# Performance work log

Hardware: AMD Instinct MI355X
Metric: run time of the kernel (lower is better)

Reference implementation:

```python
import jax, jax.numpy as jnp
import numpy as np

N_NODES = 50000
N_EDGES = 500000
IN_FEATS = 64
H_FEATS = 128
NUM_CLASSES = 4
NUM_GRAPHS = 8
NODES_PER_GRAPH = N_NODES // NUM_GRAPHS


def setup_inputs() -> dict:
    key = jax.random.key(0)
    ks = jax.random.split(key, 12)
    in_feat = jax.random.normal(ks[0], (N_NODES, IN_FEATS), dtype=jnp.float32)
    e_weight = jax.random.uniform(ks[1], (N_EDGES,), dtype=jnp.float32)
    src = jax.random.randint(ks[2], (N_EDGES,), 0, N_NODES)
    dst = jax.random.randint(ks[3], (N_EDGES,), 0, N_NODES)
    batch_num_nodes = jnp.full((NUM_GRAPHS,), NODES_PER_GRAPH, dtype=jnp.int64)
    target_node = jax.random.randint(ks[4], (NUM_GRAPHS,), 0, NODES_PER_GRAPH)
    # Glorot-style init for GraphConv weights, zero bias (DGL defaults)
    def glorot(k, fan_in, fan_out):
        s = jnp.sqrt(6.0 / (fan_in + fan_out))
        return jax.random.uniform(k, (fan_in, fan_out), minval=-s, maxval=s, dtype=jnp.float32)
    W1 = glorot(ks[5], IN_FEATS, H_FEATS)
    b1 = jnp.zeros((H_FEATS,), dtype=jnp.float32)
    W2 = glorot(ks[6], H_FEATS, H_FEATS)
    b2 = jnp.zeros((H_FEATS,), dtype=jnp.float32)
    W3 = glorot(ks[7], H_FEATS, NUM_CLASSES)
    b3 = jnp.zeros((NUM_CLASSES,), dtype=jnp.float32)
    return {"in_feat": in_feat, "e_weight": e_weight, "src": src, "dst": dst,
            "batch_num_nodes": batch_num_nodes, "target_node": target_node,
            "W1": W1, "b1": b1, "W2": W2, "b2": b2, "W3": W3, "b3": b3}


def _graph_conv(h, src, dst, e_weight, W, b, out_norm, in_norm, n_nodes):
    # DGL GraphConv, norm='both', with per-edge weights:
    # h_src scaled by out_deg^-1/2, weighted sum over edges into dst,
    # scaled by in_deg^-1/2, then dense transform + bias.
    h = h * out_norm[:, None]
    msg = h[src] * e_weight[:, None]           # [E, d] gather + scale
    agg = jax.ops.segment_sum(msg, dst, num_segments=n_nodes)  # SPMM
    agg = agg * in_norm[:, None]
    return agg @ W + b


def reference(in_feat, e_weight, src, dst, batch_num_nodes, target_node,
              W1, b1, W2, b2, W3, b3):
    n = in_feat.shape[0]
    ones = jnp.ones((src.shape[0],), dtype=in_feat.dtype)
    out_deg = jnp.clip(jax.ops.segment_sum(ones, src, num_segments=n), 1.0)
    in_deg = jnp.clip(jax.ops.segment_sum(ones, dst, num_segments=n), 1.0)
    out_norm = jax.lax.rsqrt(out_deg)
    in_norm = jax.lax.rsqrt(in_deg)

    # target node offsets for batched graphs
    offsets = jnp.concatenate([jnp.zeros((1,), batch_num_nodes.dtype),
                               jnp.cumsum(batch_num_nodes)])[:-1]
    tgt = target_node + offsets

    h = jax.nn.relu(_graph_conv(in_feat, src, dst, e_weight, W1, b1, out_norm, in_norm, n))
    h = jax.nn.relu(_graph_conv(h, src, dst, e_weight, W2, b2, out_norm, in_norm, n))
    h = _graph_conv(h, src, dst, e_weight, W3, b3, out_norm, in_norm, n)
    return h[tgt]
```

## Files before the change

kernel.cpp:

```cpp
#include <hip/hip_runtime.h>

#define NND 50000
#define NED 500000
#define F0 64
#define F1 128
#define NCLS 4
#define NG 8

#define NBLK 256
#define NTHR 1024
#define EPT 2
#define NBAR 8
#define NSUB 8
#define STG 2048
#define STGN 2048
#define BMW ((NND + 31) / 32)

#define N1CAP 4096
#define N2CAP 1024
#define E1CAP 32768
#define E2CAP 8192
#define E3CAP 2048


template <typename T>
__device__ __forceinline__ void st_wt(T* p, T v) {
    __hip_atomic_store(p, v, __ATOMIC_RELAXED, __HIP_MEMORY_SCOPE_AGENT);
}

__device__ __forceinline__ bool bt(const unsigned* __restrict__ bm, int n) {
    return (bm[n >> 5] >> (n & 31)) & 1u;
}
__device__ __forceinline__ void bset(unsigned* bm, int n) {
    atomicOr(&bm[n >> 5], 1u << (n & 31));
}

__device__ __forceinline__ void load_targets(const int* __restrict__ tnode,
                                             const unsigned* __restrict__ bnn,
                                             int* t) {
    bool is64 = true;
    #pragma unroll
    for (int k = 0; k < 4; k++) if (bnn[2 * k + 1] != 0u) { is64 = false; break; }
    long long off = 0;
    #pragma unroll
    for (int g = 0; g < NG; g++) {
        t[g] = tnode[g] + (int)off;
        off += is64 ? (long long)bnn[2 * g] : (long long)(int)bnn[g];
    }
}

__device__ __forceinline__ int tgt_of(int d, const int* t) {
    int g = -1;
    #pragma unroll
    for (int k = 0; k < NG; k++) if (d == t[k]) g = k;
    return g;
}

__device__ __forceinline__ void gbar(unsigned* bar, int i) {
    asm volatile("s_waitcnt vmcnt(0)" ::: "memory");
    __syncthreads();
    if (threadIdx.x == 0) {
        unsigned* sp = bar + (size_t)(i * (NSUB + 1) + (blockIdx.x & (NSUB - 1))) * 32;
        unsigned* mp = bar + (size_t)(i * (NSUB + 1) + NSUB) * 32;
        unsigned old = __hip_atomic_fetch_add(sp, 1u, __ATOMIC_RELAXED,
                                              __HIP_MEMORY_SCOPE_AGENT);
        if (old + 1u == (unsigned)(NBLK / NSUB))
            __hip_atomic_fetch_add(mp, 1u, __ATOMIC_RELAXED, __HIP_MEMORY_SCOPE_AGENT);
        while (__hip_atomic_load(mp, __ATOMIC_RELAXED, __HIP_MEMORY_SCOPE_AGENT)
               < (unsigned)NSUB)
            __builtin_amdgcn_s_sleep(2);
    }
    __syncthreads();
}

__global__ __launch_bounds__(256) void k_init(char* ws, unsigned zw, unsigned foff, unsigned fw) {
    unsigned t = blockIdx.x * blockDim.x + threadIdx.x;
    if (t < zw) ((uint4*)ws)[t] = make_uint4(0u, 0u, 0u, 0u);
    if (t < fw) ((uint4*)(ws + foff))[t] = make_uint4(~0u, ~0u, ~0u, ~0u);
}

__global__ __launch_bounds__(NTHR) void k_main(
        const float* __restrict__ feat, const float* __restrict__ ew,
        const int* __restrict__ src, const int* __restrict__ dst,
        const int* __restrict__ tnode, const unsigned* __restrict__ bnn,
        const float* __restrict__ W1, const float* __restrict__ b1,
        const float* __restrict__ W2, const float* __restrict__ b2,
        const float* __restrict__ W3, const float* __restrict__ b3,
        float* out,
        int* idx1, int* idx2, int* node1, int* node2,
        int* list1, int* list2, int* list3,
        unsigned* cnts, unsigned* incnt, unsigned* outcnt,
        unsigned* bm1, unsigned* bm2, unsigned* bmN,
        float* agg1c, float* agg2c, float* h1c, float* h2c, unsigned* bar) {
    __shared__ unsigned s_le, s_ln, s_eb, s_nb;
    __shared__ int stage[STG];
    __shared__ int stageN[STGN];
    __shared__ float sa[8 * F1];

    const int tid = threadIdx.x;
    const int gid = blockIdx.x * NTHR + tid;
    int tg[NG]; load_targets(tnode, bnn, tg);

    {
        if (tid == 0) { s_le = 0; s_ln = 0; }
        __syncthreads();
        int base = gid * EPT;
        if (base < NED) {
            int2 d2 = *(const int2*)(dst + base);
            int dd[2] = {d2.x, d2.y};
            #pragma unroll
            for (int k = 0; k < 2; k++) {
                int d = dd[k];
                if (tgt_of(d, tg) >= 0) {
                    stage[atomicAdd(&s_le, 1u)] = base + k;
                    atomicAdd(&incnt[d], 1u);
                    int s = src[base + k];
                    bset(bmN, s);
                    if (atomicCAS(&idx2[s], -1, -2) == -1) {
                        bset(bm2, s);
                        unsigned n = atomicAdd(&s_ln, 1u);
                        stageN[n] = s;
                    }
                }
            }
        }
        __syncthreads();
        if (tid == 0) {
            s_eb = s_le ? atomicAdd(&cnts[4], s_le) : 0u;
            s_nb = s_ln ? atomicAdd(&cnts[1], s_ln) : 0u;
        }
        __syncthreads();
        for (unsigned t = tid; t < s_le; t += NTHR) {
            unsigned p = s_eb + t; if (p < E3CAP) st_wt(&list3[p], stage[t]);
        }
        for (unsigned t = tid; t < s_ln; t += NTHR) {
            int s = stageN[t]; unsigned id = s_nb + t;
            if (id < N2CAP) { st_wt(&node2[id], s); st_wt(&idx2[s], (int)id); }
            else st_wt(&idx2[s], -1);
        }
        if (blockIdx.x == 0 && tid < NG * NCLS) st_wt(&out[tid], b3[tid & 3]);
    }
    gbar(bar, 0);

    {
        if (tid == 0) { s_le = 0; s_ln = 0; }
        __syncthreads();
        int base = gid * EPT;
        if (base < NED) {
            int2 d2 = *(const int2*)(dst + base);
            int dd[2] = {d2.x, d2.y};
            #pragma unroll
            for (int k = 0; k < 2; k++) {
                int d = dd[k];
                if (bt(bm2, d) && idx2[d] >= 0) {
                    stage[atomicAdd(&s_le, 1u)] = base + k;
                    if (tgt_of(d, tg) < 0) atomicAdd(&incnt[d], 1u);
                    int s = src[base + k];
                    bset(bmN, s);
                    if (atomicCAS(&idx1[s], -1, -2) == -1) {
                        bset(bm1, s);
                        unsigned n = atomicAdd(&s_ln, 1u);
                        stageN[n] = s;
                    }
                }
            }
        }
        __syncthreads();
        if (tid == 0) {
            s_eb = s_le ? atomicAdd(&cnts[3], s_le) : 0u;
            s_nb = s_ln ? atomicAdd(&cnts[0], s_ln) : 0u;
        }
        __syncthreads();
        for (unsigned t = tid; t < s_le; t += NTHR) {
            unsigned p = s_eb + t; if (p < E2CAP) st_wt(&list2[p], stage[t]);
        }
        for (unsigned t = tid; t < s_ln; t += NTHR) {
            int s = stageN[t]; unsigned id = s_nb + t;
            if (id < N1CAP) { st_wt(&node1[id], s); st_wt(&idx1[s], (int)id); }
            else st_wt(&idx1[s], -1);
        }
    }
    gbar(bar, 1);

    {
        if (tid == 0) s_le = 0;
        __syncthreads();
        int base = gid * EPT;
        if (base < NED) {
            int2 d2 = *(const int2*)(dst + base);
            int dd[2] = {d2.x, d2.y};
            #pragma unroll
            for (int k = 0; k < 2; k++) {
                int d = dd[k];
                if (bt(bm1, d) && idx1[d] >= 0) {
                    stage[atomicAdd(&s_le, 1u)] = base + k;
                    if (idx2[d] < 0 && tgt_of(d, tg) < 0) atomicAdd(&incnt[d], 1u);
                    bset(bmN, src[base + k]);
                }
            }
        }
        __syncthreads();
        if (tid == 0) s_eb = s_le ? atomicAdd(&cnts[2], s_le) : 0u;
        __syncthreads();
        for (unsigned t = tid; t < s_le; t += NTHR) {
            unsigned p = s_eb + t; if (p < E1CAP) st_wt(&list1[p], stage[t]);
        }
    }
    gbar(bar, 2);

    {
        int base = gid * EPT;
        if (base < NED) {
            int2 s2 = *(const int2*)(src + base);
            int ss[2] = {s2.x, s2.y};
            #pragma unroll
            for (int k = 0; k < 2; k++)
                if (bt(bmN, ss[k])) atomicAdd(&outcnt[ss[k]], 1u);
        }
    }
    gbar(bar, 3);

    {
        unsigned e1 = cnts[2]; if (e1 > E1CAP) e1 = E1CAP;
        int lane = tid & 63;
        unsigned w = (unsigned)gid >> 6;
        const unsigned nw = (NBLK * NTHR) >> 6;
        for (unsigned i = w; i < e1; i += nw) {
            int e = list1[i];
            int s = src[e], d = dst[e];
            int i1 = idx1[d]; if (i1 < 0) continue;
            float wt = ew[e] * rsqrtf(fmaxf((float)outcnt[s], 1.f));
            atomicAdd(&agg1c[(size_t)i1 * F0 + lane], feat[(size_t)s * F0 + lane] * wt);
        }
    }
    gbar(bar, 4);

    {
        unsigned n1 = cnts[0]; if (n1 > N1CAP) n1 = N1CAP;
        int sub = tid >> 7, j = tid & 127;
        for (unsigned i0 = blockIdx.x * 8; i0 < n1; i0 += NBLK * 8) {
            unsigned i = i0 + sub;
            bool act = i < n1;
            if (act && j < F0) {
                int v = node1[i];
                float innorm = rsqrtf(fmaxf((float)incnt[v], 1.f));
                sa[sub * F0 + j] = agg1c[(size_t)i * F0 + j] * innorm;
            }
            __syncthreads();
            if (act) {
                float acc = b1[j];
                #pragma unroll
                for (int k = 0; k < F0; k++) acc += sa[sub * F0 + k] * W1[k * F1 + j];
                st_wt(&h1c[(size_t)i * F1 + j], fmaxf(acc, 0.f));
            }
            __syncthreads();
        }
    }
    gbar(bar, 5);

    {
        unsigned e2 = cnts[3]; if (e2 > E2CAP) e2 = E2CAP;
        int j = tid & 127;
        unsigned grp = (unsigned)gid >> 7;
        const unsigned ng = (NBLK * NTHR) >> 7;
        for (unsigned i = grp; i < e2; i += ng) {
            int e = list2[i];
            int s = src[e], d = dst[e];
            int i1 = idx1[s], i2 = idx2[d];
            if (i1 < 0 || i2 < 0) continue;
            float wt = ew[e] * rsqrtf(fmaxf((float)outcnt[s], 1.f));
            atomicAdd(&agg2c[(size_t)i2 * F1 + j], h1c[(size_t)i1 * F1 + j] * wt);
        }
    }
    gbar(bar, 6);

    {
        unsigned n2 = cnts[1]; if (n2 > N2CAP) n2 = N2CAP;
        int sub = tid >> 7, j = tid & 127;
        for (unsigned i0 = blockIdx.x * 8; i0 < n2; i0 += NBLK * 8) {
            unsigned i = i0 + sub;
            bool act = i < n2;
            if (act) {
                int v = node2[i];
                float innorm = rsqrtf(fmaxf((float)incnt[v], 1.f));
                sa[sub * F1 + j] = agg2c[(size_t)i * F1 + j] * innorm;
            }
            __syncthreads();
            if (act) {
                float acc = 0.f;
                #pragma unroll 32
                for (int k = 0; k < F1; k++) acc += sa[sub * F1 + k] * W2[k * F1 + j];
                st_wt(&h2c[(size_t)i * F1 + j], fmaxf(acc + b2[j], 0.f));
            }
            __syncthreads();
        }
    }
    gbar(bar, 7);

    {
        unsigned e3 = cnts[4]; if (e3 > E3CAP) e3 = E3CAP;
        int lane = tid & 63;
        unsigned w = (unsigned)gid >> 6;
        const unsigned nw = (NBLK * NTHR) >> 6;
        for (unsigned i = w; i < e3; i += nw) {
            int e = list3[i];
            int s = src[e], d = dst[e];
            int i2 = idx2[s]; if (i2 < 0) continue;
            int g = tgt_of(d, tg);
            float wt = ew[e] * rsqrtf(fmaxf((float)outcnt[s], 1.f))
                             * rsqrtf(fmaxf((float)incnt[d], 1.f));
            float acc0 = 0.f, acc1 = 0.f, acc2 = 0.f, acc3 = 0.f;
            #pragma unroll
            for (int half = 0; half < 2; half++) {
                int j = lane + half * 64;
                float hv = h2c[(size_t)i2 * F1 + j] * wt;
                acc0 += hv * W3[j * NCLS + 0];
                acc1 += hv * W3[j * NCLS + 1];
                acc2 += hv * W3[j * NCLS + 2];
                acc3 += hv * W3[j * NCLS + 3];
            }
            #pragma unroll
            for (int off = 32; off; off >>= 1) {
                acc0 += __shfl_down(acc0, off, 64);
                acc1 += __shfl_down(acc1, off, 64);
                acc2 += __shfl_down(acc2, off, 64);
                acc3 += __shfl_down(acc3, off, 64);
            }
            if (lane == 0) {
                atomicAdd(&out[g * NCLS + 0], acc0);
                atomicAdd(&out[g * NCLS + 1], acc1);
                atomicAdd(&out[g * NCLS + 2], acc2);
                atomicAdd(&out[g * NCLS + 3], acc3);
            }
        }
    }
}

extern "C" void kernel_launch(void* const* d_in, const int* in_sizes, int n_in,
                              void* d_out, int out_size, void* d_ws, size_t ws_size,
                              hipStream_t stream) {
    const float* in_feat = (const float*)d_in[0];
    const float* ew      = (const float*)d_in[1];
    const int*   src     = (const int*)d_in[2];
    const int*   dst     = (const int*)d_in[3];
    const unsigned* bnn  = (const unsigned*)d_in[4];
    const int*   tnode   = (const int*)d_in[5];
    const float* W1 = (const float*)d_in[6];
    const float* b1 = (const float*)d_in[7];
    const float* W2 = (const float*)d_in[8];
    const float* b2 = (const float*)d_in[9];
    const float* W3 = (const float*)d_in[10];
    const float* b3 = (const float*)d_in[11];
    float* out = (float*)d_out;
    (void)in_sizes; (void)n_in; (void)out_size; (void)ws_size;

    char* ws = (char*)d_ws;
    size_t o = 0;
    auto alloc = [&](size_t bytes) { size_t r = o; o += (bytes + 255) & ~(size_t)255; return r; };

    size_t off_outcnt = alloc((size_t)NND * 4);
    size_t off_incnt  = alloc((size_t)NND * 4);
    size_t off_cnts   = alloc(8 * 4);
    size_t off_bar    = alloc((size_t)NBAR * (NSUB + 1) * 32 * 4);
    size_t off_bm1    = alloc((size_t)BMW * 4);
    size_t off_bm2    = alloc((size_t)BMW * 4);
    size_t off_bmN    = alloc((size_t)BMW * 4);
    size_t off_agg1   = alloc((size_t)N1CAP * F0 * 4);
    size_t off_agg2   = alloc((size_t)N2CAP * F1 * 4);
    size_t zero_bytes = o;
    size_t ff_start = o;
    size_t off_idx2   = alloc((size_t)NND * 4);
    size_t off_idx1   = alloc((size_t)NND * 4);
    size_t ff_bytes = o - ff_start;
    size_t off_node2   = alloc((size_t)N2CAP * 4);
    size_t off_node1   = alloc((size_t)N1CAP * 4);
    size_t off_list3   = alloc((size_t)E3CAP * 4);
    size_t off_list2   = alloc((size_t)E2CAP * 4);
    size_t off_list1   = alloc((size_t)E1CAP * 4);
    size_t off_h1      = alloc((size_t)N1CAP * F1 * 4);
    size_t off_h2      = alloc((size_t)N2CAP * F1 * 4);

    unsigned* outcnt  = (unsigned*)(ws + off_outcnt);
    unsigned* incnt   = (unsigned*)(ws + off_incnt);
    unsigned* cnts    = (unsigned*)(ws + off_cnts);
    unsigned* bar     = (unsigned*)(ws + off_bar);
    unsigned* bm1     = (unsigned*)(ws + off_bm1);
    unsigned* bm2     = (unsigned*)(ws + off_bm2);
    unsigned* bmN     = (unsigned*)(ws + off_bmN);
    float*    agg1c   = (float*)(ws + off_agg1);
    float*    agg2c   = (float*)(ws + off_agg2);
    int*      idx2    = (int*)(ws + off_idx2);
    int*      idx1    = (int*)(ws + off_idx1);
    int*      node2   = (int*)(ws + off_node2);
    int*      node1   = (int*)(ws + off_node1);
    int*      list3   = (int*)(ws + off_list3);
    int*      list2   = (int*)(ws + off_list2);
    int*      list1   = (int*)(ws + off_list1);
    float*    h1c     = (float*)(ws + off_h1);
    float*    h2c     = (float*)(ws + off_h2);

    unsigned zw = (unsigned)(zero_bytes / 16);
    unsigned fw = (unsigned)(ff_bytes / 16);
    unsigned iw = zw > fw ? zw : fw;
    k_init<<<(iw + 255) / 256, 256, 0, stream>>>(ws, zw, (unsigned)ff_start, fw);

    k_main<<<NBLK, NTHR, 0, stream>>>(in_feat, ew, src, dst, tnode, bnn,
                                      W1, b1, W2, b2, W3, b3, out,
                                      idx1, idx2, node1, node2,
                                      list1, list2, list3,
                                      cnts, incnt, outcnt, bm1, bm2, bmN,
                                      agg1c, agg2c, h1c, h2c, bar);
}
```

Before: 75.49 us.

## Fuse dense transforms into edge aggregation passes, dropping node-transform phases and barriers

```diff
diff --git a/kernel.cpp b/kernel.cpp
--- a/kernel.cpp
+++ b/kernel.cpp
@@ -15,6 +15,7 @@
 #define STG 2048
 #define STGN 2048
 #define BMW ((NND + 31) / 32)
+#define EMASK 0x7FFFFu
 
 #define N1CAP 4096
 #define N2CAP 1024
@@ -68,7 +69,7 @@
             __hip_atomic_fetch_add(mp, 1u, __ATOMIC_RELAXED, __HIP_MEMORY_SCOPE_AGENT);
         while (__hip_atomic_load(mp, __ATOMIC_RELAXED, __HIP_MEMORY_SCOPE_AGENT)
                < (unsigned)NSUB)
-            __builtin_amdgcn_s_sleep(2);
+            __builtin_amdgcn_s_sleep(1);
     }
     __syncthreads();
 }
@@ -87,18 +88,18 @@
         const float* __restrict__ W2, const float* __restrict__ b2,
         const float* __restrict__ W3, const float* __restrict__ b3,
         float* out,
-        int* idx1, int* idx2, int* node1, int* node2,
-        int* list1, int* list2, int* list3,
+        int* idx1, int* idx2,
+        unsigned* list1, unsigned* list2, unsigned* list3,
         unsigned* cnts, unsigned* incnt, unsigned* outcnt,
         unsigned* bm1, unsigned* bm2, unsigned* bmN,
-        float* agg1c, float* agg2c, float* h1c, float* h2c, unsigned* bar) {
+        float* agg1c, float* agg2c, unsigned* bar) {
     __shared__ unsigned s_le, s_ln, s_eb, s_nb;
-    __shared__ int stage[STG];
+    __shared__ unsigned stage[STG];
     __shared__ int stageN[STGN];
-    __shared__ float sa[8 * F1];
 
     const int tid = threadIdx.x;
     const int gid = blockIdx.x * NTHR + tid;
+    const int lane = tid & 63;
     int tg[NG]; load_targets(tnode, bnn, tg);
 
     {
@@ -111,15 +112,16 @@
             #pragma unroll
             for (int k = 0; k < 2; k++) {
                 int d = dd[k];
-                if (tgt_of(d, tg) >= 0) {
-                    stage[atomicAdd(&s_le, 1u)] = base + k;
+                int g = tgt_of(d, tg);
+                if (g >= 0) {
+                    int e = base + k;
+                    stage[atomicAdd(&s_le, 1u)] = ((unsigned)g << 19) | (unsigned)e;
                     atomicAdd(&incnt[d], 1u);
-                    int s = src[base + k];
+                    int s = src[e];
                     bset(bmN, s);
                     if (atomicCAS(&idx2[s], -1, -2) == -1) {
                         bset(bm2, s);
-                        unsigned n = atomicAdd(&s_ln, 1u);
-                        stageN[n] = s;
+                        stageN[atomicAdd(&s_ln, 1u)] = s;
                     }
                 }
             }
@@ -135,8 +137,7 @@
         }
         for (unsigned t = tid; t < s_ln; t += NTHR) {
             int s = stageN[t]; unsigned id = s_nb + t;
-            if (id < N2CAP) { st_wt(&node2[id], s); st_wt(&idx2[s], (int)id); }
-            else st_wt(&idx2[s], -1);
+            st_wt(&idx2[s], id < N2CAP ? (int)id : -1);
         }
         if (blockIdx.x == 0 && tid < NG * NCLS) st_wt(&out[tid], b3[tid & 3]);
     }
@@ -152,15 +153,18 @@
             #pragma unroll
             for (int k = 0; k < 2; k++) {
                 int d = dd[k];
-                if (bt(bm2, d) && idx2[d] >= 0) {
-                    stage[atomicAdd(&s_le, 1u)] = base + k;
-                    if (tgt_of(d, tg) < 0) atomicAdd(&incnt[d], 1u);
-                    int s = src[base + k];
-                    bset(bmN, s);
-                    if (atomicCAS(&idx1[s], -1, -2) == -1) {
-                        bset(bm1, s);
-                        unsigned n = atomicAdd(&s_ln, 1u);
-                        stageN[n] = s;
+                if (bt(bm2, d)) {
+                    int iv = idx2[d];
+                    if (iv >= 0) {
+                        int e = base + k;
+                        stage[atomicAdd(&s_le, 1u)] = ((unsigned)iv << 19) | (unsigned)e;
+                        if (tgt_of(d, tg) < 0) atomicAdd(&incnt[d], 1u);
+                        int s = src[e];
+                        bset(bmN, s);
+                        if (atomicCAS(&idx1[s], -1, -2) == -1) {
+                            bset(bm1, s);
+                            stageN[atomicAdd(&s_ln, 1u)] = s;
+                        }
                     }
                 }
             }
@@ -176,8 +180,7 @@
         }
         for (unsigned t = tid; t < s_ln; t += NTHR) {
             int s = stageN[t]; unsigned id = s_nb + t;
-            if (id < N1CAP) { st_wt(&node1[id], s); st_wt(&idx1[s], (int)id); }
-            else st_wt(&idx1[s], -1);
+            st_wt(&idx1[s], id < N1CAP ? (int)id : -1);
         }
     }
     gbar(bar, 1);
@@ -192,10 +195,14 @@
             #pragma unroll
             for (int k = 0; k < 2; k++) {
                 int d = dd[k];
-                if (bt(bm1, d) && idx1[d] >= 0) {
-                    stage[atomicAdd(&s_le, 1u)] = base + k;
-                    if (idx2[d] < 0 && tgt_of(d, tg) < 0) atomicAdd(&incnt[d], 1u);
-                    bset(bmN, src[base + k]);
+                if (bt(bm1, d)) {
+                    int iv = idx1[d];
+                    if (iv >= 0) {
+                        int e = base + k;
+                        stage[atomicAdd(&s_le, 1u)] = ((unsigned)iv << 19) | (unsigned)e;
+                        if (idx2[d] < 0 && tgt_of(d, tg) < 0) atomicAdd(&incnt[d], 1u);
+                        bset(bmN, src[e]);
+                    }
                 }
             }
         }
@@ -222,115 +229,101 @@
 
     {
         unsigned e1 = cnts[2]; if (e1 > E1CAP) e1 = E1CAP;
-        int lane = tid & 63;
         unsigned w = (unsigned)gid >> 6;
         const unsigned nw = (NBLK * NTHR) >> 6;
-        for (unsigned i = w; i < e1; i += nw) {
-            int e = list1[i];
-            int s = src[e], d = dst[e];
-            int i1 = idx1[d]; if (i1 < 0) continue;
-            float wt = ew[e] * rsqrtf(fmaxf((float)outcnt[s], 1.f));
-            atomicAdd(&agg1c[(size_t)i1 * F0 + lane], feat[(size_t)s * F0 + lane] * wt);
+        for (unsigned i = w; i < e1; i += 2 * nw) {
+            unsigned pk0 = list1[i];
+            unsigned j2 = i + nw;
+            unsigned pk1 = (j2 < e1) ? list1[j2] : 0u;
+            int e0 = pk0 & EMASK, i10 = pk0 >> 19;
+            float we0 = ew[e0]; int s0 = src[e0];
+            int e1i = pk1 & EMASK, i11 = pk1 >> 19;
+            float we1 = 0.f; int s1 = 0;
+            if (j2 < e1) { we1 = ew[e1i]; s1 = src[e1i]; }
+            float wt0 = we0 * rsqrtf(fmaxf((float)outcnt[s0], 1.f));
+            atomicAdd(&agg1c[(size_t)i10 * F0 + lane],
+                      feat[(size_t)s0 * F0 + lane] * wt0);
+            if (j2 < e1) {
+                float wt1 = we1 * rsqrtf(fmaxf((float)outcnt[s1], 1.f));
+                atomicAdd(&agg1c[(size_t)i11 * F0 + lane],
+                          feat[(size_t)s1 * F0 + lane] * wt1);
+            }
         }
     }
     gbar(bar, 4);
 
     {
-        unsigned n1 = cnts[0]; if (n1 > N1CAP) n1 = N1CAP;
-        int sub = tid >> 7, j = tid & 127;
-        for (unsigned i0 = blockIdx.x * 8; i0 < n1; i0 += NBLK * 8) {
-            unsigned i = i0 + sub;
-            bool act = i < n1;
-            if (act && j < F0) {
-                int v = node1[i];
-                float innorm = rsqrtf(fmaxf((float)incnt[v], 1.f));
-                sa[sub * F0 + j] = agg1c[(size_t)i * F0 + j] * innorm;
-            }
-            __syncthreads();
-            if (act) {
-                float acc = b1[j];
-                #pragma unroll
-                for (int k = 0; k < F0; k++) acc += sa[sub * F0 + k] * W1[k * F1 + j];
-                st_wt(&h1c[(size_t)i * F1 + j], fmaxf(acc, 0.f));
-            }
-            __syncthreads();
+        unsigned e2 = cnts[3]; if (e2 > E2CAP) e2 = E2CAP;
+        unsigned w = (unsigned)gid >> 6;
+        const unsigned nw = (NBLK * NTHR) >> 6;
+        for (unsigned i = w; i < e2; i += nw) {
+            unsigned pk = list2[i];
+            int e = pk & EMASK, i2 = pk >> 19;
+            float we = ew[e]; int s = src[e];
+            int i1 = idx1[s]; if (i1 < 0) continue;
+            float wt = we * rsqrtf(fmaxf((float)outcnt[s], 1.f));
+            float innorm1 = rsqrtf(fmaxf((float)incnt[s], 1.f));
+            float rv = agg1c[(size_t)i1 * F0 + lane];
+            float acc0 = 0.f, acc1 = 0.f;
+            #pragma unroll 8
+            for (int k2 = 0; k2 < F0; k2++) {
+                float bv = __shfl(rv, k2, 64);
+                acc0 += bv * W1[k2 * F1 + lane];
+                acc1 += bv * W1[k2 * F1 + lane + 64];
+            }
+            float h0 = fmaxf(acc0 * innorm1 + b1[lane], 0.f) * wt;
+            float h1v = fmaxf(acc1 * innorm1 + b1[lane + 64], 0.f) * wt;
+            atomicAdd(&agg2c[(size_t)i2 * F1 + lane], h0);
+            atomicAdd(&agg2c[(size_t)i2 * F1 + lane + 64], h1v);
         }
     }
     gbar(bar, 5);
 
     {
-        unsigned e2 = cnts[3]; if (e2 > E2CAP) e2 = E2CAP;
-        int j = tid & 127;
-        unsigned grp = (unsigned)gid >> 7;
-        const unsigned ng = (NBLK * NTHR) >> 7;
-        for (unsigned i = grp; i < e2; i += ng) {
-            int e = list2[i];
-            int s = src[e], d = dst[e];
-            int i1 = idx1[s], i2 = idx2[d];
-            if (i1 < 0 || i2 < 0) continue;
-            float wt = ew[e] * rsqrtf(fmaxf((float)outcnt[s], 1.f));
-            atomicAdd(&agg2c[(size_t)i2 * F1 + j], h1c[(size_t)i1 * F1 + j] * wt);
-        }
-    }
-    gbar(bar, 6);
-
-    {
-        unsigned n2 = cnts[1]; if (n2 > N2CAP) n2 = N2CAP;
-        int sub = tid >> 7, j = tid & 127;
-        for (unsigned i0 = blockIdx.x * 8; i0 < n2; i0 += NBLK * 8) {
-            unsigned i = i0 + sub;
-            bool act = i < n2;
-            if (act) {
-                int v = node2[i];
-                float innorm = rsqrtf(fmaxf((float)incnt[v], 1.f));
-                sa[sub * F1 + j] = agg2c[(size_t)i * F1 + j] * innorm;
-            }
-            __syncthreads();
-            if (act) {
-                float acc = 0.f;
-                #pragma unroll 32
-                for (int k = 0; k < F1; k++) acc += sa[sub * F1 + k] * W2[k * F1 + j];
-                st_wt(&h2c[(size_t)i * F1 + j], fmaxf(acc + b2[j], 0.f));
-            }
-            __syncthreads();
-        }
-    }
-    gbar(bar, 7);
-
-    {
         unsigned e3 = cnts[4]; if (e3 > E3CAP) e3 = E3CAP;
-        int lane = tid & 63;
         unsigned w = (unsigned)gid >> 6;
         const unsigned nw = (NBLK * NTHR) >> 6;
         for (unsigned i = w; i < e3; i += nw) {
-            int e = list3[i];
-            int s = src[e], d = dst[e];
+            unsigned pk = list3[i];
+            int e = pk & EMASK, g = pk >> 19;
+            float we = ew[e]; int s = src[e];
             int i2 = idx2[s]; if (i2 < 0) continue;
-            int g = tgt_of(d, tg);
-            float wt = ew[e] * rsqrtf(fmaxf((float)outcnt[s], 1.f))
-                             * rsqrtf(fmaxf((float)incnt[d], 1.f));
-            float acc0 = 0.f, acc1 = 0.f, acc2 = 0.f, acc3 = 0.f;
-            #pragma unroll
-            for (int half = 0; half < 2; half++) {
-                int j = lane + half * 64;
-                float hv = h2c[(size_t)i2 * F1 + j] * wt;
-                acc0 += hv * W3[j * NCLS + 0];
-                acc1 += hv * W3[j * NCLS + 1];
-                acc2 += hv * W3[j * NCLS + 2];
-                acc3 += hv * W3[j * NCLS + 3];
-            }
+            float wt = we * rsqrtf(fmaxf((float)outcnt[s], 1.f))
+                          * rsqrtf(fmaxf((float)incnt[tg[g]], 1.f));
+            float innorm2 = rsqrtf(fmaxf((float)incnt[s], 1.f));
+            float rv0 = agg2c[(size_t)i2 * F1 + lane];
+            float rv1 = agg2c[(size_t)i2 * F1 + lane + 64];
+            float acc0 = 0.f, acc1 = 0.f;
+            #pragma unroll 8
+            for (int k2 = 0; k2 < 64; k2++) {
+                float bv = __shfl(rv0, k2, 64);
+                acc0 += bv * W2[k2 * F1 + lane];
+                acc1 += bv * W2[k2 * F1 + lane + 64];
+            }
+            #pragma unroll 8
+            for (int k2 = 0; k2 < 64; k2++) {
+                float bv = __shfl(rv1, k2, 64);
+                acc0 += bv * W2[(k2 + 64) * F1 + lane];
+                acc1 += bv * W2[(k2 + 64) * F1 + lane + 64];
+            }
+            float h20 = fmaxf(acc0 * innorm2 + b2[lane], 0.f);
+            float h21 = fmaxf(acc1 * innorm2 + b2[lane + 64], 0.f);
+            float oc0 = (h20 * W3[lane * NCLS + 0] + h21 * W3[(lane + 64) * NCLS + 0]) * wt;
+            float oc1 = (h20 * W3[lane * NCLS + 1] + h21 * W3[(lane + 64) * NCLS + 1]) * wt;
+            float oc2 = (h20 * W3[lane * NCLS + 2] + h21 * W3[(lane + 64) * NCLS + 2]) * wt;
+            float oc3 = (h20 * W3[lane * NCLS + 3] + h21 * W3[(lane + 64) * NCLS + 3]) * wt;
             #pragma unroll
             for (int off = 32; off; off >>= 1) {
-                acc0 += __shfl_down(acc0, off, 64);
-                acc1 += __shfl_down(acc1, off, 64);
-                acc2 += __shfl_down(acc2, off, 64);
-                acc3 += __shfl_down(acc3, off, 64);
+                oc0 += __shfl_down(oc0, off, 64);
+                oc1 += __shfl_down(oc1, off, 64);
+                oc2 += __shfl_down(oc2, off, 64);
+                oc3 += __shfl_down(oc3, off, 64);
             }
             if (lane == 0) {
-                atomicAdd(&out[g * NCLS + 0], acc0);
-                atomicAdd(&out[g * NCLS + 1], acc1);
-                atomicAdd(&out[g * NCLS + 2], acc2);
-                atomicAdd(&out[g * NCLS + 3], acc3);
+                atomicAdd(&out[g * NCLS + 0], oc0);
+                atomicAdd(&out[g * NCLS + 1], oc1);
+                atomicAdd(&out[g * NCLS + 2], oc2);
+                atomicAdd(&out[g * NCLS + 3], oc3);
             }
         }
     }
@@ -372,13 +365,9 @@
     size_t off_idx2   = alloc((size_t)NND * 4);
     size_t off_idx1   = alloc((size_t)NND * 4);
     size_t ff_bytes = o - ff_start;
-    size_t off_node2   = alloc((size_t)N2CAP * 4);
-    size_t off_node1   = alloc((size_t)N1CAP * 4);
     size_t off_list3   = alloc((size_t)E3CAP * 4);
     size_t off_list2   = alloc((size_t)E2CAP * 4);
     size_t off_list1   = alloc((size_t)E1CAP * 4);
-    size_t off_h1      = alloc((size_t)N1CAP * F1 * 4);
-    size_t off_h2      = alloc((size_t)N2CAP * F1 * 4);
 
     unsigned* outcnt  = (unsigned*)(ws + off_outcnt);
     unsigned* incnt   = (unsigned*)(ws + off_incnt);
@@ -391,13 +380,9 @@
     float*    agg2c   = (float*)(ws + off_agg2);
     int*      idx2    = (int*)(ws + off_idx2);
     int*      idx1    = (int*)(ws + off_idx1);
-    int*      node2   = (int*)(ws + off_node2);
-    int*      node1   = (int*)(ws + off_node1);
-    int*      list3   = (int*)(ws + off_list3);
-    int*      list2   = (int*)(ws + off_list2);
-    int*      list1   = (int*)(ws + off_list1);
-    float*    h1c     = (float*)(ws + off_h1);
-    float*    h2c     = (float*)(ws + off_h2);
+    unsigned* list3   = (unsigned*)(ws + off_list3);
+    unsigned* list2   = (unsigned*)(ws + off_list2);
+    unsigned* list1   = (unsigned*)(ws + off_list1);
 
     unsigned zw = (unsigned)(zero_bytes / 16);
     unsigned fw = (unsigned)(ff_bytes / 16);
@@ -406,8 +391,7 @@
 
     k_main<<<NBLK, NTHR, 0, stream>>>(in_feat, ew, src, dst, tnode, bnn,
                                       W1, b1, W2, b2, W3, b3, out,
-                                      idx1, idx2, node1, node2,
-                                      list1, list2, list3,
+                                      idx1, idx2, list1, list2, list3,
                                       cnts, incnt, outcnt, bm1, bm2, bmN,
-                                      agg1c, agg2c, h1c, h2c, bar);
-}
+                                      agg1c, agg2c, bar);
+}
```

Result: faster. 61.87 us (-18.0%).
